# Performance work log

Hardware: AMD Instinct MI355X
Metric: run time of the kernel (lower is better)

Reference implementation:

```python
import jax, jax.numpy as jnp
import numpy as np

N_NODES = 50000
N_EDGES = 600000
N_GRAPHS = 64
HID = 128
NLAYERS = 4
IN_DIM = 5
NCLS = 5
EPS = 1e-5


def setup_inputs() -> dict:
    key = jax.random.key(0)
    ks = jax.random.split(key, 16)
    x = jax.random.normal(ks[0], (N_NODES, IN_DIM), dtype=jnp.float32)
    edge_index = jax.random.randint(ks[1], (2, N_EDGES), 0, N_NODES, dtype=jnp.int64)
    batch = jnp.sort(jax.random.randint(ks[2], (N_NODES,), 0, N_GRAPHS, dtype=jnp.int64))
    s = 0.05
    Wp = jax.random.normal(ks[3], (IN_DIM, HID), jnp.float32) * s
    bp = jnp.zeros((HID,), jnp.float32)
    Wg = jax.random.normal(ks[4], (NLAYERS, HID, HID), jnp.float32) * s
    bg = jnp.zeros((NLAYERS, HID), jnp.float32)
    gamma = jnp.ones((NLAYERS, HID), jnp.float32)
    beta = jnp.zeros((NLAYERS, HID), jnp.float32)
    W1 = jax.random.normal(ks[5], (2 * HID, HID), jnp.float32) * s
    b1 = jnp.zeros((HID,), jnp.float32)
    W2 = jax.random.normal(ks[6], (HID, HID // 2), jnp.float32) * s
    b2 = jnp.zeros((HID // 2,), jnp.float32)
    W3 = jax.random.normal(ks[7], (HID // 2, NCLS), jnp.float32) * s
    b3 = jnp.zeros((NCLS,), jnp.float32)
    return {"x": x, "edge_index": edge_index, "batch": batch, "Wp": Wp, "bp": bp,
            "Wg": Wg, "bg": bg, "gamma": gamma, "beta": beta,
            "W1": W1, "b1": b1, "W2": W2, "b2": b2, "W3": W3, "b3": b3}


def reference(x, edge_index, batch, Wp, bp, Wg, bg, gamma, beta, W1, b1, W2, b2, W3, b3):
    N = x.shape[0]
    # GCN with added self-loops and symmetric normalization (PyG GCNConv defaults)
    loop = jnp.arange(N)
    src = jnp.concatenate([edge_index[0], loop])
    dst = jnp.concatenate([edge_index[1], loop])
    deg = jax.ops.segment_sum(jnp.ones_like(dst, dtype=x.dtype), dst, num_segments=N)
    dinv = jax.lax.rsqrt(deg)  # deg >= 1 thanks to self-loops
    norm = dinv[src] * dinv[dst]  # [E+N]
    h = x @ Wp + bp  # [N, HID]
    for i in range(NLAYERS):
        m = h @ Wg[i]
        agg = jax.ops.segment_sum(m[src] * norm[:, None], dst, num_segments=N) + bg[i]
        # BatchNorm1d (training-mode stats over nodes)
        mu = jnp.mean(agg, axis=0)
        var = jnp.var(agg, axis=0)
        h = gamma[i] * (agg - mu) * jax.lax.rsqrt(var + EPS) + beta[i]
        h = jax.nn.relu(h)  # dropout is identity in eval mode
    # mean_max global pooling per graph
    cnt = jax.ops.segment_sum(jnp.ones((N,), h.dtype), batch, num_segments=N_GRAPHS)
    x_mean = jax.ops.segment_sum(h, batch, num_segments=N_GRAPHS) / jnp.maximum(cnt, 1.0)[:, None]
    x_max = jax.ops.segment_max(h, batch, num_segments=N_GRAPHS)
    x_max = jnp.where(jnp.isfinite(x_max), x_max, 0.0)
    pooled = jnp.concatenate([x_mean, x_max], axis=1)  # [B, 2*HID]
    h1 = jax.nn.relu(pooled @ W1 + b1)
    h2 = jax.nn.relu(h1 @ W2 + b2)
    return h2 @ W3 + b3  # [B, num_classes]
```

## Files before the change

### kernel.cpp

```cpp
#include <hip/hip_runtime.h>
#include <hip/hip_bf16.h>

#define N_NODES 50000
#define N_EDGES 600000
#define N_GRAPHS 64
#define HID 128
#define NLAYERS 4
#define IN_DIM 5
#define NCLS 5
#define EPS 1e-5f
#define SCAN_BLK ((N_NODES + 511) / 512)
#define FILL_BLK ((N_EDGES + 255) / 256)
#define POOL_CHUNKS 16
#define BSLOT 64
#define WS 136

typedef __attribute__((ext_vector_type(8))) short s16x8;
typedef __attribute__((ext_vector_type(4))) float f32x4;

__device__ __forceinline__ unsigned short f2bf(float x) {
    unsigned u = __float_as_uint(x);
    unsigned r = (u + 0x7fffu + ((u >> 16) & 1u)) >> 16;
    return (unsigned short)r;
}
__device__ __forceinline__ float2 bfpair(unsigned u) {
    float2 r;
    r.x = __uint_as_float(u << 16);
    r.y = __uint_as_float(u & 0xffff0000u);
    return r;
}
__device__ __forceinline__ float bf2f(unsigned short s) {
    return __uint_as_float(((unsigned)s) << 16);
}


__global__ void k_count(const int* __restrict__ dst, int* __restrict__ cnt) {
    int i = blockIdx.x * blockDim.x + threadIdx.x;
    if (i < N_EDGES) atomicAdd(&cnt[dst[i]], 1);
}

__global__ void k_scan1(const int* __restrict__ cnt, int* __restrict__ rp, int* __restrict__ bsum) {
    __shared__ int s[512];
    int t = threadIdx.x;
    int i = blockIdx.x * 512 + t;
    int v = (i < N_NODES) ? cnt[i] : 0;
    s[t] = v;
    __syncthreads();
    for (int off = 1; off < 512; off <<= 1) {
        int x = (t >= off) ? s[t - off] : 0;
        __syncthreads();
        s[t] += x;
        __syncthreads();
    }
    if (i < N_NODES) rp[i + 1] = s[t];
    if (t == 511) bsum[blockIdx.x] = s[511];
}

__global__ void k_scan2g(int* __restrict__ bsum, const int* __restrict__ batch,
                         int* __restrict__ gstart) {
    if (blockIdx.x == 0) {
        __shared__ int s[128];
        int t = threadIdx.x;
        int v = (t < SCAN_BLK) ? bsum[t] : 0;
        s[t] = v;
        __syncthreads();
        for (int off = 1; off < 128; off <<= 1) {
            int x = (t >= off) ? s[t - off] : 0;
            __syncthreads();
            s[t] += x;
            __syncthreads();
        }
        if (t < SCAN_BLK) bsum[t] = s[t] - v;
    } else {
        int t = threadIdx.x;
        if (t <= N_GRAPHS) {
            int lo = 0, hi = N_NODES;
            while (lo < hi) {
                int mid = (lo + hi) >> 1;
                if (batch[mid] < t) lo = mid + 1; else hi = mid;
            }
            gstart[t] = lo;
        }
    }
}

__global__ void k_scan3d(int* __restrict__ rp, const int* __restrict__ bsum,
                         const int* __restrict__ cnt, float* __restrict__ dinv,
                         int* __restrict__ cursor) {
    int i = blockIdx.x * 512 + threadIdx.x;
    if (i < N_NODES) {
        int c = cnt[i];
        int incl = rp[i + 1] + bsum[blockIdx.x];
        rp[i + 1] = incl;
        cursor[i] = incl - c;
        dinv[i] = rsqrtf((float)(c + 1));
    }
    if (i == 0) rp[0] = 0;
}

__global__ void k_fillw(const int* __restrict__ src, const int* __restrict__ dst,
                        int* __restrict__ cursor, int* __restrict__ cwc,
                        const float* __restrict__ Wg, unsigned short* __restrict__ WtG) {
    int b = blockIdx.x;
    if (b < FILL_BLK) {
        int e = b * 256 + threadIdx.x;
        if (e < N_EDGES) {
            int d = dst[e];
            int pos = atomicAdd(&cursor[d], 1);
            cwc[pos] = src[e];
        }
    } else {
        int idx = (b - FILL_BLK) * 256 + threadIdx.x;
        int l = idx >> 14;
        int r = idx & 16383;
        int n = r >> 7, k = r & 127;
        WtG[idx] = f2bf(Wg[l * HID * HID + k * HID + n]);
    }
}


__global__ __launch_bounds__(256, 3) void k_gemmM(const unsigned short* __restrict__ Abf,
                                                  const float* __restrict__ x,
                                                  const float* __restrict__ Wp,
                                                  const float* __restrict__ bp,
                                                  const unsigned short* __restrict__ WtG,
                                                  unsigned short* __restrict__ Bm,
                                                  const float* __restrict__ psum,
                                                  const float* __restrict__ psq,
                                                  const float* __restrict__ gamma,
                                                  const float* __restrict__ beta,
                                                  int layer0) {
    __shared__ unsigned short Wt[HID * WS];
    __shared__ unsigned short Al[64 * WS];
    __shared__ float scl[HID], shf[HID];
    int t = threadIdx.x;
    {
        const uint4* Wg4 = (const uint4*)WtG;
        for (int idx = t; idx < HID * 16; idx += 256) {
            int n = idx >> 4, c = idx & 15;
            *(uint4*)&Wt[n * WS + c * 8] = Wg4[idx];
        }
    }
    if (!layer0 && t < HID) {
        float s = 0.f, s2 = 0.f;
#pragma unroll 8
        for (int b = 0; b < BSLOT; b++) {
            s += psum[b * HID + t];
            s2 += psq[b * HID + t];
        }
        const float invN = 1.f / (float)N_NODES;
        float mu = s * invN;
        float var = s2 * invN - mu * mu;
        float rs = rsqrtf(var + EPS) * gamma[t];
        scl[t] = rs;
        shf[t] = beta[t] - mu * rs;
    }
    int lane = t & 63, wv = t >> 6;
    int rbase = (wv & 1) * 32;
    int cbase = (wv >> 1) * 64;
    int mr = lane & 15, q = lane >> 4;
    const int numTiles = (N_NODES + 63) / 64;
    for (int tile = blockIdx.x; tile < numTiles; tile += gridDim.x) {
        int n0 = tile * 64;
        int limRow = min(64, N_NODES - n0);
        __syncthreads();
        if (layer0) {
            for (int idx = t; idx < 64 * HID; idx += 256) {
                int n = idx >> 7, k = idx & 127;
                int node = n0 + n;
                float acc = 0.f;
                if (node < N_NODES) {
                    acc = bp[k];
#pragma unroll
                    for (int j = 0; j < IN_DIM; j++) acc += x[node * IN_DIM + j] * Wp[j * HID + k];
                }
                Al[n * WS + k] = f2bf(acc);
            }
        } else {
            const uint2* Ag = (const uint2*)(Abf + (size_t)n0 * HID);
            for (int idx = t; idx < 64 * 32; idx += 256) {
                int row = idx >> 5, c4 = idx & 31;
                uint2 u = (row < limRow) ? Ag[row * 32 + c4] : make_uint2(0u, 0u);
                float2 ab = bfpair(u.x);
                float2 cd = bfpair(u.y);
                int kf = c4 * 4;
                float4 sc = *(const float4*)&scl[kf];
                float4 sh = *(const float4*)&shf[kf];
                float v0 = fmaxf(ab.x * sc.x + sh.x, 0.f);
                float v1 = fmaxf(ab.y * sc.y + sh.y, 0.f);
                float v2 = fmaxf(cd.x * sc.z + sh.z, 0.f);
                float v3 = fmaxf(cd.y * sc.w + sh.w, 0.f);
                unsigned lo = (unsigned)f2bf(v0) | ((unsigned)f2bf(v1) << 16);
                unsigned hi = (unsigned)f2bf(v2) | ((unsigned)f2bf(v3) << 16);
                *(uint2*)&Al[row * WS + kf] = make_uint2(lo, hi);
            }
        }
        __syncthreads();
        f32x4 acc[2][4];
#pragma unroll
        for (int rt = 0; rt < 2; rt++)
#pragma unroll
            for (int ct = 0; ct < 4; ct++) acc[rt][ct] = (f32x4){0.f, 0.f, 0.f, 0.f};
#pragma unroll
        for (int kk = 0; kk < HID; kk += 32) {
            s16x8 a0 = *(const s16x8*)&Al[(rbase + mr) * WS + kk + q * 8];
            s16x8 a1 = *(const s16x8*)&Al[(rbase + 16 + mr) * WS + kk + q * 8];
#pragma unroll
            for (int ct = 0; ct < 4; ct++) {
                s16x8 b = *(const s16x8*)&Wt[(cbase + ct * 16 + mr) * WS + kk + q * 8];
                acc[0][ct] = __builtin_amdgcn_mfma_f32_16x16x32_bf16(a0, b, acc[0][ct], 0, 0, 0);
                acc[1][ct] = __builtin_amdgcn_mfma_f32_16x16x32_bf16(a1, b, acc[1][ct], 0, 0, 0);
            }
        }
        __syncthreads();
#pragma unroll
        for (int rt = 0; rt < 2; rt++)
#pragma unroll
            for (int ct = 0; ct < 4; ct++)
#pragma unroll
                for (int r = 0; r < 4; r++) {
                    int rloc = rbase + rt * 16 + q * 4 + r;
                    int f = cbase + ct * 16 + mr;
                    Al[rloc * WS + f] = f2bf(acc[rt][ct][r]);
                }
        __syncthreads();
        for (int idx = t; idx < 64 * 16; idx += 256) {
            int row = idx >> 4, c = idx & 15;
            if (row < limRow)
                *(uint4*)&Bm[(size_t)(n0 + row) * HID + c * 8] = *(const uint4*)&Al[row * WS + c * 8];
        }
    }
}


__global__ __launch_bounds__(256) void k_gather(const uint4* __restrict__ Bm4,
                                                const int* __restrict__ rp,
                                                const int* __restrict__ cwc,
                                                const float* __restrict__ dinv,
                                                const float* __restrict__ bg,
                                                unsigned short* __restrict__ Aout,
                                                float* __restrict__ psum,
                                                float* __restrict__ psq) {
    __shared__ float ls[4 * HID], lq[4 * HID];
    int wave = threadIdx.x >> 6;
    int lane = threadIdx.x & 63;
    int s = lane & 15;
    int p = lane >> 4;
    int f = s * 8;
    int v = blockIdx.x * 16 + wave * 4 + p;
    int beg = rp[v], end = rp[v + 1];
    float dv = dinv[v];
    float a0, a1, a2, a3, a4, a5, a6, a7;
    {
        uint4 u = Bm4[(size_t)v * 16 + s];
        float2 q0 = bfpair(u.x), q1 = bfpair(u.y), q2 = bfpair(u.z), q3 = bfpair(u.w);
        a0 = q0.x * dv; a1 = q0.y * dv; a2 = q1.x * dv; a3 = q1.y * dv;
        a4 = q2.x * dv; a5 = q2.y * dv; a6 = q3.x * dv; a7 = q3.y * dv;
    }
    int e = beg;
    for (; e + 1 < end; e += 2) {
        int c0 = cwc[e];
        int c1 = cwc[e + 1];
        uint4 u0 = Bm4[(size_t)c0 * 16 + s];
        uint4 u1 = Bm4[(size_t)c1 * 16 + s];
        float w0 = dinv[c0];
        float w1 = dinv[c1];
        float2 x0 = bfpair(u0.x), x1 = bfpair(u0.y), x2 = bfpair(u0.z), x3 = bfpair(u0.w);
        float2 y0 = bfpair(u1.x), y1 = bfpair(u1.y), y2 = bfpair(u1.z), y3 = bfpair(u1.w);
        a0 += x0.x * w0 + y0.x * w1;
        a1 += x0.y * w0 + y0.y * w1;
        a2 += x1.x * w0 + y1.x * w1;
        a3 += x1.y * w0 + y1.y * w1;
        a4 += x2.x * w0 + y2.x * w1;
        a5 += x2.y * w0 + y2.y * w1;
        a6 += x3.x * w0 + y3.x * w1;
        a7 += x3.y * w0 + y3.y * w1;
    }
    if (e < end) {
        int c0 = cwc[e];
        uint4 u = Bm4[(size_t)c0 * 16 + s];
        float w = dinv[c0];
        float2 x0 = bfpair(u.x), x1 = bfpair(u.y), x2 = bfpair(u.z), x3 = bfpair(u.w);
        a0 += x0.x * w; a1 += x0.y * w; a2 += x1.x * w; a3 += x1.y * w;
        a4 += x2.x * w; a5 += x2.y * w; a6 += x3.x * w; a7 += x3.y * w;
    }
    float r0 = a0 * dv + bg[f + 0];
    float r1 = a1 * dv + bg[f + 1];
    float r2 = a2 * dv + bg[f + 2];
    float r3 = a3 * dv + bg[f + 3];
    float r4 = a4 * dv + bg[f + 4];
    float r5 = a5 * dv + bg[f + 5];
    float r6 = a6 * dv + bg[f + 6];
    float r7 = a7 * dv + bg[f + 7];
    unsigned short b0 = f2bf(r0), b1 = f2bf(r1), b2 = f2bf(r2), b3 = f2bf(r3);
    unsigned short b4 = f2bf(r4), b5 = f2bf(r5), b6 = f2bf(r6), b7 = f2bf(r7);
    uint4 o;
    o.x = (unsigned)b0 | ((unsigned)b1 << 16);
    o.y = (unsigned)b2 | ((unsigned)b3 << 16);
    o.z = (unsigned)b4 | ((unsigned)b5 << 16);
    o.w = (unsigned)b6 | ((unsigned)b7 << 16);
    *(uint4*)&Aout[(size_t)v * HID + f] = o;
    float v0 = bf2f(b0), v1 = bf2f(b1), v2 = bf2f(b2), v3 = bf2f(b3);
    float v4 = bf2f(b4), v5 = bf2f(b5), v6 = bf2f(b6), v7 = bf2f(b7);
    float ts0 = v0, ts1 = v1, ts2 = v2, ts3 = v3;
    float ts4 = v4, ts5 = v5, ts6 = v6, ts7 = v7;
    float tq0 = v0 * v0, tq1 = v1 * v1, tq2 = v2 * v2, tq3 = v3 * v3;
    float tq4 = v4 * v4, tq5 = v5 * v5, tq6 = v6 * v6, tq7 = v7 * v7;
    ts0 += __shfl_xor(ts0, 16); ts1 += __shfl_xor(ts1, 16);
    ts2 += __shfl_xor(ts2, 16); ts3 += __shfl_xor(ts3, 16);
    ts4 += __shfl_xor(ts4, 16); ts5 += __shfl_xor(ts5, 16);
    ts6 += __shfl_xor(ts6, 16); ts7 += __shfl_xor(ts7, 16);
    tq0 += __shfl_xor(tq0, 16); tq1 += __shfl_xor(tq1, 16);
    tq2 += __shfl_xor(tq2, 16); tq3 += __shfl_xor(tq3, 16);
    tq4 += __shfl_xor(tq4, 16); tq5 += __shfl_xor(tq5, 16);
    tq6 += __shfl_xor(tq6, 16); tq7 += __shfl_xor(tq7, 16);
    ts0 += __shfl_xor(ts0, 32); ts1 += __shfl_xor(ts1, 32);
    ts2 += __shfl_xor(ts2, 32); ts3 += __shfl_xor(ts3, 32);
    ts4 += __shfl_xor(ts4, 32); ts5 += __shfl_xor(ts5, 32);
    ts6 += __shfl_xor(ts6, 32); ts7 += __shfl_xor(ts7, 32);
    tq0 += __shfl_xor(tq0, 32); tq1 += __shfl_xor(tq1, 32);
    tq2 += __shfl_xor(tq2, 32); tq3 += __shfl_xor(tq3, 32);
    tq4 += __shfl_xor(tq4, 32); tq5 += __shfl_xor(tq5, 32);
    tq6 += __shfl_xor(tq6, 32); tq7 += __shfl_xor(tq7, 32);
    if (p == 0) {
        float* lsw = &ls[wave * HID + f];
        float* lqw = &lq[wave * HID + f];
        lsw[0] = ts0; lsw[1] = ts1; lsw[2] = ts2; lsw[3] = ts3;
        lsw[4] = ts4; lsw[5] = ts5; lsw[6] = ts6; lsw[7] = ts7;
        lqw[0] = tq0; lqw[1] = tq1; lqw[2] = tq2; lqw[3] = tq3;
        lqw[4] = tq4; lqw[5] = tq5; lqw[6] = tq6; lqw[7] = tq7;
    }
    __syncthreads();
    int tt = threadIdx.x;
    if (tt < HID) {
        float ssum = ls[tt] + ls[HID + tt] + ls[2 * HID + tt] + ls[3 * HID + tt];
        float ssq = lq[tt] + lq[HID + tt] + lq[2 * HID + tt] + lq[3 * HID + tt];
        int slot = blockIdx.x & (BSLOT - 1);
        atomicAdd(&psum[slot * HID + tt], ssum);
        atomicAdd(&psq[slot * HID + tt], ssq);
    }
}


__global__ __launch_bounds__(128) void k_pool(const unsigned short* __restrict__ A,
                                              const float* __restrict__ psum,
                                              const float* __restrict__ psq,
                                              const float* __restrict__ gamma,
                                              const float* __restrict__ beta,
                                              const int* __restrict__ gstart,
                                              float* __restrict__ poolPart) {
    int g = blockIdx.x;
    int c = blockIdx.y;
    int f = threadIdx.x;
    float s = 0.f, s2 = 0.f;
#pragma unroll 8
    for (int b = 0; b < BSLOT; b++) {
        s += psum[b * HID + f];
        s2 += psq[b * HID + f];
    }
    const float invN = 1.f / (float)N_NODES;
    float mu = s * invN;
    float var = s2 * invN - mu * mu;
    float sc = rsqrtf(var + EPS) * gamma[f];
    float sh = beta[f] - mu * sc;
    int beg = gstart[g], end = gstart[g + 1];
    int len = end - beg;
    int per = (len + POOL_CHUNKS - 1) / POOL_CHUNKS;
    int s0 = beg + c * per;
    int s1 = min(s0 + per, end);
    float sa = 0.f, sb = 0.f, ma = 0.f, mb = 0.f;
    int n = s0;
    for (; n + 1 < s1; n += 2) {
        float v0 = bf2f(A[(size_t)n * HID + f]);
        float v1 = bf2f(A[(size_t)(n + 1) * HID + f]);
        v0 = fmaxf(v0 * sc + sh, 0.f);
        v1 = fmaxf(v1 * sc + sh, 0.f);
        sa += v0; ma = fmaxf(ma, v0);
        sb += v1; mb = fmaxf(mb, v1);
    }
    if (n < s1) {
        float v = fmaxf(bf2f(A[(size_t)n * HID + f]) * sc + sh, 0.f);
        sa += v; ma = fmaxf(ma, v);
    }
    poolPart[((size_t)g * POOL_CHUNKS + c) * 256 + f] = sa + sb;
    poolPart[((size_t)g * POOL_CHUNKS + c) * 256 + 128 + f] = fmaxf(ma, mb);
}


__global__ __launch_bounds__(128) void k_head(const float* __restrict__ poolPart,
                                              const int* __restrict__ gstart,
                                              const float* __restrict__ W1, const float* __restrict__ b1,
                                              const float* __restrict__ W2, const float* __restrict__ b2,
                                              const float* __restrict__ W3, const float* __restrict__ b3,
                                              float* __restrict__ out) {
    __shared__ float pl[2 * HID];
    __shared__ float h1[HID];
    __shared__ float h2[HID / 2];
    int g = blockIdx.x, t = threadIdx.x;
    float cnt = fmaxf((float)(gstart[g + 1] - gstart[g]), 1.f);
    float s = 0.f, mx = 0.f;
#pragma unroll
    for (int c = 0; c < POOL_CHUNKS; c++) {
        const float* p = &poolPart[((size_t)g * POOL_CHUNKS + c) * 256];
        s += p[t];
        mx = fmaxf(mx, p[128 + t]);
    }
    pl[t] = s / cnt;
    pl[HID + t] = mx;
    __syncthreads();
    float acc = b1[t];
    for (int k = 0; k < 2 * HID; k++) acc += pl[k] * W1[k * HID + t];
    h1[t] = fmaxf(acc, 0.f);
    __syncthreads();
    if (t < HID / 2) {
        float a2 = b2[t];
        for (int k = 0; k < HID; k++) a2 += h1[k] * W2[k * (HID / 2) + t];
        h2[t] = fmaxf(a2, 0.f);
    }
    __syncthreads();
    if (t < NCLS) {
        float a3 = b3[t];
        for (int k = 0; k < HID / 2; k++) a3 += h2[k] * W3[k * NCLS + t];
        out[g * NCLS + t] = a3;
    }
}

extern "C" void kernel_launch(void* const* d_in, const int* in_sizes, int n_in,
                              void* d_out, int out_size, void* d_ws, size_t ws_size,
                              hipStream_t stream) {
    const float* x     = (const float*)d_in[0];
    const int*   ei    = (const int*)d_in[1];
    const int*   batch = (const int*)d_in[2];
    const float* Wp    = (const float*)d_in[3];
    const float* bp    = (const float*)d_in[4];
    const float* Wg    = (const float*)d_in[5];
    const float* bg    = (const float*)d_in[6];
    const float* gamma = (const float*)d_in[7];
    const float* beta  = (const float*)d_in[8];
    const float* W1    = (const float*)d_in[9];
    const float* b1    = (const float*)d_in[10];
    const float* W2    = (const float*)d_in[11];
    const float* b2    = (const float*)d_in[12];
    const float* W3    = (const float*)d_in[13];
    const float* b3    = (const float*)d_in[14];
    const int* src = ei;
    const int* dst = ei + N_EDGES;
    float* out = (float*)d_out;

    char* base = (char*)d_ws;
    size_t off = 0;
    auto alloc = [&](size_t bytes) -> void* {
        void* p = base + off;
        off += (bytes + 255) & ~(size_t)255;
        return p;
    };
    int*   counts = (int*)alloc((size_t)N_NODES * 4);
    float* psum   = (float*)alloc((size_t)NLAYERS * BSLOT * HID * 4);
    float* psq    = (float*)alloc((size_t)NLAYERS * BSLOT * HID * 4);
    size_t zeroBytes = off;
    int*   cursor  = (int*)alloc((size_t)N_NODES * 4);
    int*   rp      = (int*)alloc((size_t)(N_NODES + 1) * 4);
    int*   bsum    = (int*)alloc(128 * 4);
    int*   cwc     = (int*)alloc((size_t)N_EDGES * 4);
    float* dinv    = (float*)alloc((size_t)N_NODES * 4);
    int*   gstart  = (int*)alloc((size_t)(N_GRAPHS + 1) * 4);
    float* poolPart= (float*)alloc((size_t)N_GRAPHS * POOL_CHUNKS * 256 * 4);
    unsigned short* WtG = (unsigned short*)alloc((size_t)NLAYERS * HID * HID * 2);
    unsigned short* A = (unsigned short*)alloc((size_t)N_NODES * HID * 2);
    unsigned short* B = (unsigned short*)alloc((size_t)N_NODES * HID * 2);
    (void)ws_size; (void)in_sizes; (void)n_in; (void)out_size;

    hipMemsetAsync(d_ws, 0, zeroBytes, stream);

    k_count<<<(N_EDGES + 255) / 256, 256, 0, stream>>>(dst, counts);
    k_scan1<<<SCAN_BLK, 512, 0, stream>>>(counts, rp, bsum);
    k_scan2g<<<2, 128, 0, stream>>>(bsum, batch, gstart);
    k_scan3d<<<SCAN_BLK, 512, 0, stream>>>(rp, bsum, counts, dinv, cursor);
    k_fillw<<<(N_EDGES + 255) / 256 + (NLAYERS * HID * HID) / 256, 256, 0, stream>>>(
        src, dst, cursor, cwc, Wg, WtG);

    for (int i = 0; i < NLAYERS; i++) {
        int pl = (i == 0) ? 0 : (i - 1);
        k_gemmM<<<768, 256, 0, stream>>>(A, x, Wp, bp, WtG + (size_t)i * HID * HID, B,
                                         psum + (size_t)pl * BSLOT * HID,
                                         psq + (size_t)pl * BSLOT * HID,
                                         gamma + pl * HID, beta + pl * HID,
                                         (i == 0) ? 1 : 0);
        k_gather<<<N_NODES / 16, 256, 0, stream>>>((const uint4*)B, rp, cwc, dinv,
                                                   bg + i * HID, A,
                                                   psum + (size_t)i * BSLOT * HID,
                                                   psq + (size_t)i * BSLOT * HID);
    }
    dim3 pg(N_GRAPHS, POOL_CHUNKS);
    k_pool<<<pg, 128, 0, stream>>>(A, psum + (size_t)3 * BSLOT * HID,
                                   psq + (size_t)3 * BSLOT * HID,
                                   gamma + 3 * HID, beta + 3 * HID, gstart, poolPart);
    k_head<<<N_GRAPHS, 128, 0, stream>>>(poolPart, gstart, W1, b1, W2, b2, W3, b3, out);
}
```

Measured before the change: 375.3 us.

## Build CSR via 64-node buckets with shared-memory local sort

Replaces the count/three-pass scan/atomic-fill CSR construction with a bucketed approach. Edges are first scattered into fixed-capacity per-bucket buffers, packed as src<<6 | local dst, using one atomic per edge on a small counter array. A single-block scan then computes bucket bases, and each bucket is counted and placed in LDS to emit row pointers, dinv and the column array. This cuts the launch count and spreads global atomics differently, but adds an extra pass over the edges and assumes no bucket exceeds 1024 edges and that src fits in 26 bits.

New measurement: 464.3 us. 23.7% more time.

```diff
diff --git a/kernel.cpp b/kernel.cpp
--- a/kernel.cpp
+++ b/kernel.cpp
@@ -9,11 +9,14 @@
 #define IN_DIM 5
 #define NCLS 5
 #define EPS 1e-5f
-#define SCAN_BLK ((N_NODES + 511) / 512)
-#define FILL_BLK ((N_EDGES + 255) / 256)
 #define POOL_CHUNKS 16
 #define BSLOT 64
 #define WS 136
+
+#define NBUCK ((N_NODES + 63) / 64)
+#define BCAP 1024
+#define EDGE_BLK ((N_EDGES + 255) / 256)
+#define WT_BLK ((NLAYERS * HID * HID) / 256)
 
 typedef __attribute__((ext_vector_type(8))) short s16x8;
 typedef __attribute__((ext_vector_type(4))) float f32x4;
@@ -34,45 +37,21 @@
 }
 
 
-__global__ void k_count(const int* __restrict__ dst, int* __restrict__ cnt) {
-    int i = blockIdx.x * blockDim.x + threadIdx.x;
-    if (i < N_EDGES) atomicAdd(&cnt[dst[i]], 1);
-}
-
-__global__ void k_scan1(const int* __restrict__ cnt, int* __restrict__ rp, int* __restrict__ bsum) {
-    __shared__ int s[512];
-    int t = threadIdx.x;
-    int i = blockIdx.x * 512 + t;
-    int v = (i < N_NODES) ? cnt[i] : 0;
-    s[t] = v;
-    __syncthreads();
-    for (int off = 1; off < 512; off <<= 1) {
-        int x = (t >= off) ? s[t - off] : 0;
-        __syncthreads();
-        s[t] += x;
-        __syncthreads();
-    }
-    if (i < N_NODES) rp[i + 1] = s[t];
-    if (t == 511) bsum[blockIdx.x] = s[511];
-}
-
-__global__ void k_scan2g(int* __restrict__ bsum, const int* __restrict__ batch,
-                         int* __restrict__ gstart) {
-    if (blockIdx.x == 0) {
-        __shared__ int s[128];
-        int t = threadIdx.x;
-        int v = (t < SCAN_BLK) ? bsum[t] : 0;
-        s[t] = v;
-        __syncthreads();
-        for (int off = 1; off < 128; off <<= 1) {
-            int x = (t >= off) ? s[t - off] : 0;
-            __syncthreads();
-            s[t] += x;
-            __syncthreads();
-        }
-        if (t < SCAN_BLK) bsum[t] = s[t] - v;
-    } else {
-        int t = threadIdx.x;
+__global__ void k_bucket(const int* __restrict__ src, const int* __restrict__ dst,
+                         const int* __restrict__ batch, const float* __restrict__ Wg,
+                         int* __restrict__ bcur, unsigned* __restrict__ ebuf,
+                         int* __restrict__ gstart, unsigned short* __restrict__ WtG) {
+    int b = blockIdx.x, t = threadIdx.x;
+    if (b < EDGE_BLK) {
+        int e = b * 256 + t;
+        if (e < N_EDGES) {
+            int d = dst[e];
+            int s = src[e];
+            int bk = d >> 6;
+            int pos = atomicAdd(&bcur[bk], 1);
+            ebuf[bk * BCAP + pos] = ((unsigned)s << 6) | (unsigned)(d & 63);
+        }
+    } else if (b == EDGE_BLK) {
         if (t <= N_GRAPHS) {
             int lo = 0, hi = N_NODES;
             while (lo < hi) {
@@ -81,40 +60,80 @@
             }
             gstart[t] = lo;
         }
-    }
-}
-
-__global__ void k_scan3d(int* __restrict__ rp, const int* __restrict__ bsum,
-                         const int* __restrict__ cnt, float* __restrict__ dinv,
-                         int* __restrict__ cursor) {
-    int i = blockIdx.x * 512 + threadIdx.x;
-    if (i < N_NODES) {
-        int c = cnt[i];
-        int incl = rp[i + 1] + bsum[blockIdx.x];
-        rp[i + 1] = incl;
-        cursor[i] = incl - c;
-        dinv[i] = rsqrtf((float)(c + 1));
-    }
-    if (i == 0) rp[0] = 0;
-}
-
-__global__ void k_fillw(const int* __restrict__ src, const int* __restrict__ dst,
-                        int* __restrict__ cursor, int* __restrict__ cwc,
-                        const float* __restrict__ Wg, unsigned short* __restrict__ WtG) {
-    int b = blockIdx.x;
-    if (b < FILL_BLK) {
-        int e = b * 256 + threadIdx.x;
-        if (e < N_EDGES) {
-            int d = dst[e];
-            int pos = atomicAdd(&cursor[d], 1);
-            cwc[pos] = src[e];
-        }
     } else {
-        int idx = (b - FILL_BLK) * 256 + threadIdx.x;
+        int idx = (b - EDGE_BLK - 1) * 256 + t;
         int l = idx >> 14;
         int r = idx & 16383;
         int n = r >> 7, k = r & 127;
         WtG[idx] = f2bf(Wg[l * HID * HID + k * HID + n]);
+    }
+}
+
+
+__global__ __launch_bounds__(1024) void k_bscan(const int* __restrict__ bcur,
+                                                int* __restrict__ bbase,
+                                                int* __restrict__ rp) {
+    __shared__ int s[1024];
+    int t = threadIdx.x;
+    int v = (t < NBUCK) ? bcur[t] : 0;
+    s[t] = v;
+    __syncthreads();
+    for (int off = 1; off < 1024; off <<= 1) {
+        int x = (t >= off) ? s[t - off] : 0;
+        __syncthreads();
+        s[t] += x;
+        __syncthreads();
+    }
+    if (t < NBUCK) bbase[t] = s[t] - v;
+    if (t == NBUCK - 1) {
+        bbase[NBUCK] = s[t];
+        rp[N_NODES] = s[t];
+    }
+}
+
+
+__global__ __launch_bounds__(256) void k_bsort(const unsigned* __restrict__ ebuf,
+                                               const int* __restrict__ bcur,
+                                               const int* __restrict__ bbase,
+                                               int* __restrict__ rp,
+                                               float* __restrict__ dinv,
+                                               int* __restrict__ cwc) {
+    __shared__ unsigned le[BCAP];
+    __shared__ int cnt[64];
+    __shared__ int sc[64];
+    __shared__ int cur[64];
+    int b = blockIdx.x, t = threadIdx.x;
+    int sz = bcur[b];
+    int base = bbase[b];
+    int n0 = b * 64;
+    for (int i = t; i < sz; i += 256) le[i] = ebuf[b * BCAP + i];
+    if (t < 64) cnt[t] = 0;
+    __syncthreads();
+    for (int i = t; i < sz; i += 256) atomicAdd(&cnt[le[i] & 63u], 1);
+    __syncthreads();
+    int vc = (t < 64) ? cnt[t] : 0;
+    if (t < 64) sc[t] = vc;
+    __syncthreads();
+    for (int off = 1; off < 64; off <<= 1) {
+        int x = (t < 64 && t >= off) ? sc[t - off] : 0;
+        __syncthreads();
+        if (t < 64) sc[t] += x;
+        __syncthreads();
+    }
+    if (t < 64) {
+        int excl = sc[t] - vc;
+        cur[t] = excl;
+        int node = n0 + t;
+        if (node < N_NODES) {
+            rp[node] = base + excl;
+            dinv[node] = rsqrtf((float)(vc + 1));
+        }
+    }
+    __syncthreads();
+    for (int i = t; i < sz; i += 256) {
+        unsigned u = le[i];
+        int p = atomicAdd(&cur[u & 63u], 1);
+        cwc[base + p] = (int)(u >> 6);
     }
 }
 
@@ -454,13 +473,13 @@
         off += (bytes + 255) & ~(size_t)255;
         return p;
     };
-    int*   counts = (int*)alloc((size_t)N_NODES * 4);
+    int*   bcur   = (int*)alloc((size_t)NBUCK * 4);
     float* psum   = (float*)alloc((size_t)NLAYERS * BSLOT * HID * 4);
     float* psq    = (float*)alloc((size_t)NLAYERS * BSLOT * HID * 4);
     size_t zeroBytes = off;
-    int*   cursor  = (int*)alloc((size_t)N_NODES * 4);
+    unsigned* ebuf = (unsigned*)alloc((size_t)NBUCK * BCAP * 4);
+    int*   bbase   = (int*)alloc((size_t)(NBUCK + 1) * 4);
     int*   rp      = (int*)alloc((size_t)(N_NODES + 1) * 4);
-    int*   bsum    = (int*)alloc(128 * 4);
     int*   cwc     = (int*)alloc((size_t)N_EDGES * 4);
     float* dinv    = (float*)alloc((size_t)N_NODES * 4);
     int*   gstart  = (int*)alloc((size_t)(N_GRAPHS + 1) * 4);
@@ -472,12 +491,10 @@
 
     hipMemsetAsync(d_ws, 0, zeroBytes, stream);
 
-    k_count<<<(N_EDGES + 255) / 256, 256, 0, stream>>>(dst, counts);
-    k_scan1<<<SCAN_BLK, 512, 0, stream>>>(counts, rp, bsum);
-    k_scan2g<<<2, 128, 0, stream>>>(bsum, batch, gstart);
-    k_scan3d<<<SCAN_BLK, 512, 0, stream>>>(rp, bsum, counts, dinv, cursor);
-    k_fillw<<<(N_EDGES + 255) / 256 + (NLAYERS * HID * HID) / 256, 256, 0, stream>>>(
-        src, dst, cursor, cwc, Wg, WtG);
+    k_bucket<<<EDGE_BLK + 1 + WT_BLK, 256, 0, stream>>>(src, dst, batch, Wg, bcur,
+                                                        ebuf, gstart, WtG);
+    k_bscan<<<1, 1024, 0, stream>>>(bcur, bbase, rp);
+    k_bsort<<<NBUCK, 256, 0, stream>>>(ebuf, bcur, bbase, rp, dinv, cwc);
 
     for (int i = 0; i < NLAYERS; i++) {
         int pl = (i == 0) ? 0 : (i - 1);
```
